# Performance work log

Measured on AMD Instinct MI355X. Metric: run time of the kernel, lower is better.

Reference implementation:

```python
import jax, jax.numpy as jnp
import numpy as np

N_NODES = 100000


def _graph_conv(x, W, b, src, dst, n_nodes):
    # DGL GraphConv, norm='both':
    #   h = x * out_deg(src)^{-1/2}; h = h @ W; agg = scatter_sum over dst;
    #   out = agg * in_deg(dst)^{-1/2} + b
    ones = jnp.ones(src.shape, dtype=x.dtype)
    out_deg = jax.ops.segment_sum(ones, src, num_segments=n_nodes)
    in_deg = jax.ops.segment_sum(ones, dst, num_segments=n_nodes)
    norm_src = jax.lax.rsqrt(jnp.maximum(out_deg, 1.0))  # [N]
    norm_dst = jax.lax.rsqrt(jnp.maximum(in_deg, 1.0))   # [N]
    h = (x * norm_src[:, None]) @ W                      # [N, hid]
    msgs = h[src]                                        # [E, hid] gather
    agg = jax.ops.segment_sum(msgs, dst, num_segments=n_nodes)  # [N, hid]
    return jax.nn.relu(agg * norm_dst[:, None] + b)


def setup_inputs() -> dict:
    key = jax.random.key(0)
    k1, k2, k3, k4, k5 = jax.random.split(key, 5)
    n, e, d = N_NODES, 1600000, 128
    x = jax.random.normal(k1, (n, d), dtype=jnp.float32)
    src = jax.random.randint(k2, (e,), 0, n, dtype=jnp.int32)
    dst = jax.random.randint(k3, (e,), 0, n, dtype=jnp.int32)
    # Xavier-ish init for GraphConv weights, zero bias (DGL default)
    W1 = jax.random.normal(k4, (d, d), dtype=jnp.float32) / np.sqrt(d)
    W2 = jax.random.normal(k5, (d, d), dtype=jnp.float32) / np.sqrt(d)
    b1 = jnp.zeros((d,), dtype=jnp.float32)
    b2 = jnp.zeros((d,), dtype=jnp.float32)
    return {"x": x, "W1": W1, "b1": b1, "W2": W2, "b2": b2, "src": src, "dst": dst}


def reference(x, W1, b1, W2, b2, src, dst):
    h = _graph_conv(x, W1, b1, src, dst, N_NODES)
    h = _graph_conv(h, W2, b2, src, dst, N_NODES)
    return h
```

## Files before the change

kernel.cpp:

```cpp
#include <hip/hip_runtime.h>
#include <hip/hip_fp16.h>

#define HD 128
#define CHUNK 4096
#define MAXNB 512

typedef _Float16 f16x8 __attribute__((ext_vector_type(8)));
typedef float f32x4 __attribute__((ext_vector_type(4)));

__global__ __launch_bounds__(256) void hist_count(const int* __restrict__ src,
                                                  const int* __restrict__ dst,
                                                  unsigned int* __restrict__ cnt4s,
                                                  unsigned int* __restrict__ gHist,
                                                  int N, int NB, int NC, int E) {
    __shared__ unsigned int hist[MAXNB];
    for (int b = threadIdx.x; b < NB; b += 256) hist[b] = 0;
    __syncthreads();
    int base = blockIdx.x * CHUNK;
    int e0 = base + 4 * threadIdx.x;
#pragma unroll
    for (int it = 0; it < CHUNK / 1024; ++it, e0 += 1024) {
        if (e0 + 3 < E) {
            int4 s4 = *(const int4*)(src + e0);
            int4 d4 = *(const int4*)(dst + e0);
            atomicAdd(&cnt4s[0 * N + s4.x], 1u);
            atomicAdd(&cnt4s[1 * N + s4.y], 1u);
            atomicAdd(&cnt4s[2 * N + s4.z], 1u);
            atomicAdd(&cnt4s[3 * N + s4.w], 1u);
            atomicAdd(&hist[d4.x >> 8], 1u);
            atomicAdd(&hist[d4.y >> 8], 1u);
            atomicAdd(&hist[d4.z >> 8], 1u);
            atomicAdd(&hist[d4.w >> 8], 1u);
        } else {
            for (int j = 0; j < 4; ++j)
                if (e0 + j < E) {
                    atomicAdd(&cnt4s[j * N + src[e0 + j]], 1u);
                    atomicAdd(&hist[dst[e0 + j] >> 8], 1u);
                }
        }
    }
    __syncthreads();
    for (int b = threadIdx.x; b < NB; b += 256)
        gHist[(size_t)b * NC + blockIdx.x] = hist[b];
}

__global__ __launch_bounds__(256) void make_norm_src(const unsigned int* __restrict__ cnt4s,
                                                     float* __restrict__ norm_src, int N) {
    int i = blockIdx.x * 256 + threadIdx.x;
    if (i < N) {
        float od = (float)(cnt4s[i] + cnt4s[N + i] + cnt4s[2 * N + i] + cnt4s[3 * N + i]);
        norm_src[i] = rsqrtf(od > 1.f ? od : 1.f);
    }
}

__global__ __launch_bounds__(256) void prep_w(const float* __restrict__ W1,
                                              const float* __restrict__ W2,
                                              _Float16* __restrict__ Wt) {
    const float* W = blockIdx.x ? W2 : W1;
    _Float16* T = Wt + (size_t)blockIdx.x * HD * HD;
    for (int i = threadIdx.x; i < HD * HD; i += 256) {
        int k = i >> 7, c = i & 127;
        T[c * HD + k] = (_Float16)W[i];
    }
}

__global__ __launch_bounds__(256) void scan_a(const unsigned int* __restrict__ cnt,
                                              unsigned int* __restrict__ excl,
                                              unsigned int* __restrict__ bsum, int n) {
    int i = blockIdx.x * 256 + threadIdx.x;
    unsigned int v = (i < n) ? cnt[i] : 0u;
    unsigned int x = v;
#pragma unroll
    for (int d = 1; d < 64; d <<= 1) {
        unsigned int y = __shfl_up(x, d, 64);
        if ((threadIdx.x & 63) >= d) x += y;
    }
    __shared__ unsigned int wsum[4];
    if ((threadIdx.x & 63) == 63) wsum[threadIdx.x >> 6] = x;
    __syncthreads();
    unsigned int woff = 0;
    for (int w = 0; w < (int)(threadIdx.x >> 6); ++w) woff += wsum[w];
    unsigned int incl = x + woff;
    if (i < n) excl[i] = incl - v;
    if (threadIdx.x == 255) bsum[blockIdx.x] = incl;
}

__global__ __launch_bounds__(1024) void scan_b(const unsigned int* __restrict__ bsum,
                                               unsigned int* __restrict__ boff, int nb) {
    int t = threadIdx.x;
    unsigned int v = (t < nb) ? bsum[t] : 0u;
    unsigned int x = v;
#pragma unroll
    for (int d = 1; d < 64; d <<= 1) {
        unsigned int y = __shfl_up(x, d, 64);
        if ((t & 63) >= d) x += y;
    }
    __shared__ unsigned int wsum[16];
    if ((t & 63) == 63) wsum[t >> 6] = x;
    __syncthreads();
    unsigned int woff = 0;
    for (int w = 0; w < (t >> 6); ++w) woff += wsum[w];
    unsigned int incl = x + woff;
    if (t < nb) boff[t] = incl - v;
}

__global__ __launch_bounds__(256) void scan_c(unsigned int* __restrict__ excl,
                                              const unsigned int* __restrict__ boff, int n) {
    int i = blockIdx.x * 256 + threadIdx.x;
    if (i < n) excl[i] += boff[blockIdx.x];
}

__global__ __launch_bounds__(256) void scatter_coarse(const int* __restrict__ src,
                                                      const int* __restrict__ dst,
                                                      const unsigned int* __restrict__ scanA,
                                                      unsigned int* __restrict__ packed,
                                                      int NB, int NC, int E) {
    __shared__ unsigned int curs[MAXNB];
    int chunk = blockIdx.x;
    for (int b = threadIdx.x; b < NB; b += 256)
        curs[b] = scanA[(size_t)b * NC + chunk];
    __syncthreads();
    int base = chunk * CHUNK;
    int end = base + CHUNK < E ? base + CHUNK : E;
    for (int e = base + threadIdx.x; e < end; e += 256) {
        int d = dst[e];
        int s = src[e];
        unsigned int pos = atomicAdd(&curs[d >> 8], 1u);
        packed[pos] = ((unsigned int)(d & 255) << 24) | (unsigned int)s;
    }
}

__global__ __launch_bounds__(256) void fine_sort(const unsigned int* __restrict__ packed,
                                                 const unsigned int* __restrict__ scanA,
                                                 int* __restrict__ sorted_src,
                                                 unsigned int* __restrict__ offsets,
                                                 unsigned int* __restrict__ cntg,
                                                 float* __restrict__ normd,
                                                 int NB, int NC, int N, int E) {
    __shared__ unsigned int cnt[256];
    __shared__ unsigned int curs[256];
    __shared__ unsigned int wsum[4];
    int b = blockIdx.x;
    int t = threadIdx.x;
    unsigned int S = scanA[(size_t)b * NC];
    unsigned int T = (b + 1 < NB) ? scanA[(size_t)(b + 1) * NC] : (unsigned int)E;
    cnt[t] = 0;
    __syncthreads();
    for (unsigned int j = S + t; j < T; j += 256)
        atomicAdd(&cnt[packed[j] >> 24], 1u);
    __syncthreads();
    unsigned int v = cnt[t], x = v;
    int lane = t & 63;
#pragma unroll
    for (int d = 1; d < 64; d <<= 1) {
        unsigned int y = __shfl_up(x, d, 64);
        if (lane >= d) x += y;
    }
    if (lane == 63) wsum[t >> 6] = x;
    __syncthreads();
    unsigned int woff = 0;
    for (int w = 0; w < (t >> 6); ++w) woff += wsum[w];
    unsigned int ex = x - v + woff;
    curs[t] = ex;
    int node = b * 256 + t;
    if (node < N) {
        offsets[node] = S + ex;
        cntg[node] = v;
        float f = (float)v;
        normd[node] = rsqrtf(f > 1.f ? f : 1.f);
    }
    __syncthreads();
    for (unsigned int j = S + t; j < T; j += 256) {
        unsigned int p = packed[j];
        unsigned int pos = S + atomicAdd(&curs[p >> 24], 1u);
        sorted_src[pos] = (int)(p & 0xFFFFFFu);
    }
}

__global__ __launch_bounds__(256) void prep_x(const float* __restrict__ x,
                                              const float* __restrict__ norm,
                                              _Float16* __restrict__ xh, int total) {
    int t = blockIdx.x * 256 + threadIdx.x;
    if (t >= total) return;
    int row = t >> 5;
    float nr = norm[row];
    float4 v = ((const float4*)x)[t];
    __half2 lo = __floats2half2_rn(v.x * nr, v.y * nr);
    __half2 hi = __floats2half2_rn(v.z * nr, v.w * nr);
    uint2 pk;
    pk.x = *(unsigned int*)&lo;
    pk.y = *(unsigned int*)&hi;
    ((uint2*)xh)[t] = pk;
}

__global__ __launch_bounds__(256) void gemm_mfma(const _Float16* __restrict__ xh,
                                                 const _Float16* __restrict__ Wt,
                                                 _Float16* __restrict__ h, int n) {
    const int tid = threadIdx.x;
    const int w  = tid >> 6;
    const int l  = tid & 63;
    const int lg = l >> 4;
    const int li = l & 15;
    const int m  = blockIdx.x * 64 + w * 16 + li;

    const _Float16* xrow = xh + (size_t)m * HD + lg * 8;
    f16x8 xf[4];
#pragma unroll
    for (int kk = 0; kk < 4; ++kk)
        xf[kk] = *(const f16x8*)(xrow + kk * 32);

    f32x4 acc[8];
#pragma unroll
    for (int t = 0; t < 8; ++t) acc[t] = (f32x4){0.f, 0.f, 0.f, 0.f};

#pragma unroll
    for (int t = 0; t < 8; ++t) {
        const _Float16* wrow = Wt + (size_t)(t * 16 + li) * HD + lg * 8;
#pragma unroll
        for (int kk = 0; kk < 4; ++kk) {
            f16x8 wf = *(const f16x8*)(wrow + kk * 32);
            acc[t] = __builtin_amdgcn_mfma_f32_16x16x32_f16(wf, xf[kk], acc[t], 0, 0, 0);
        }
    }

    if (m < n) {
        _Float16* hp = h + (size_t)m * HD + lg * 4;
#pragma unroll
        for (int t = 0; t < 8; ++t) {
            __half2 p0 = __floats2half2_rn(acc[t][0], acc[t][1]);
            __half2 p1 = __floats2half2_rn(acc[t][2], acc[t][3]);
            uint2 pk;
            pk.x = *(unsigned int*)&p0;
            pk.y = *(unsigned int*)&p1;
            *(uint2*)(hp + t * 16) = pk;
        }
    }
}

template <bool MID>
__global__ __launch_bounds__(256) void aggregate_k(const __half* __restrict__ h,
                                                   const int* __restrict__ sorted_src,
                                                   const unsigned int* __restrict__ offsets,
                                                   const unsigned int* __restrict__ cnt,
                                                   const float* __restrict__ norm_dst,
                                                   const float* __restrict__ nsrc,
                                                   const float* __restrict__ bias,
                                                   float* __restrict__ outF,
                                                   __half* __restrict__ outH, int n) {
    int node = blockIdx.x * 4 + (int)(threadIdx.x >> 6);
    if (node >= n) return;
    int lane = threadIdx.x & 63;
    int g   = lane >> 4;
    int sub = lane & 15;

    unsigned int start = offsets[node];
    unsigned int deg   = cnt[node];
    const int* sp = sorted_src + start;
    const uint4* h4 = (const uint4*)h;

    float acc[8];
#pragma unroll
    for (int j = 0; j < 8; ++j) acc[j] = 0.f;

#define ACCUM(u)                                                                  \
    { float2 f;                                                                   \
      f = __half22float2(*(const __half2*)&(u).x); acc[0] += f.x; acc[1] += f.y;  \
      f = __half22float2(*(const __half2*)&(u).y); acc[2] += f.x; acc[3] += f.y;  \
      f = __half22float2(*(const __half2*)&(u).z); acc[4] += f.x; acc[5] += f.y;  \
      f = __half22float2(*(const __half2*)&(u).w); acc[6] += f.x; acc[7] += f.y; }

    unsigned int i = 0;
    for (; i + 16 <= deg; i += 16) {
        int s0 = sp[i + g];
        int s1 = sp[i + 4 + g];
        int s2 = sp[i + 8 + g];
        int s3 = sp[i + 12 + g];
        uint4 u0 = h4[(size_t)s0 * 16 + sub];
        uint4 u1 = h4[(size_t)s1 * 16 + sub];
        uint4 u2 = h4[(size_t)s2 * 16 + sub];
        uint4 u3 = h4[(size_t)s3 * 16 + sub];
        ACCUM(u0);
        ACCUM(u1);
        ACCUM(u2);
        ACCUM(u3);
    }
    for (; i < deg; i += 4) {
        if (i + g < deg) {
            int s = sp[i + g];
            uint4 u = h4[(size_t)s * 16 + sub];
            ACCUM(u);
        }
    }
#undef ACCUM

#pragma unroll
    for (int j = 0; j < 8; ++j) {
        acc[j] += __shfl_xor(acc[j], 16, 64);
        acc[j] += __shfl_xor(acc[j], 32, 64);
    }

    float nd = norm_dst[node];
    int col2 = sub * 4 + g;
    float2 bb = ((const float2*)bias)[col2];
    float vx = fmaxf(fmaf(acc[g * 2 + 0], nd, bb.x), 0.f);
    float vy = fmaxf(fmaf(acc[g * 2 + 1], nd, bb.y), 0.f);
    if (MID) {
        float ns = nsrc[node];
        __half2 p = __floats2half2_rn(vx * ns, vy * ns);
        ((__half2*)outH)[(size_t)node * 64 + col2] = p;
    } else {
        ((float2*)outF)[(size_t)node * 64 + col2] = make_float2(vx, vy);
    }
}

extern "C" void kernel_launch(void* const* d_in, const int* in_sizes, int n_in,
                              void* d_out, int out_size, void* d_ws, size_t ws_size,
                              hipStream_t stream) {
    const float* x   = (const float*)d_in[0];
    const float* W1  = (const float*)d_in[1];
    const float* b1  = (const float*)d_in[2];
    const float* W2  = (const float*)d_in[3];
    const float* b2  = (const float*)d_in[4];
    const int*   src = (const int*)d_in[5];
    const int*   dst = (const int*)d_in[6];

    const int N = in_sizes[0] / HD;
    const int E = in_sizes[5];
    float* out = (float*)d_out;

    const int NP = (N + 63) & ~63;
    const int NB = (N + 255) / 256;
    const int NC = (E + CHUNK - 1) / CHUNK;
    const int scanLen = NB * NC;
    const int nbS = (scanLen + 255) / 256;
    const int nbN = (N + 255) / 256;

    float*        norm_src = (float*)d_ws;
    float*        normd    = norm_src + N;
    unsigned int* cntg     = (unsigned int*)(normd + N);
    unsigned int* offsets  = cntg + N;
    unsigned int* cnt4s    = offsets + N;
    unsigned int* gHist    = cnt4s + 4 * N;
    unsigned int* scanA    = gHist + scanLen;
    unsigned int* bsum     = scanA + scanLen;
    unsigned int* boff     = bsum + 1024;
    unsigned int* packed   = boff + 1024;
    int*          sorted   = (int*)(packed + E);
    _Float16*     h        = (_Float16*)(sorted + E);
    _Float16*     xh       = h + (size_t)NP * HD;
    _Float16*     Wt       = xh + (size_t)NP * HD;

    hipMemsetAsync(cnt4s, 0, (size_t)4 * N * 4, stream);
    prep_w<<<2, 256, 0, stream>>>(W1, W2, Wt);
    hist_count<<<NC, 256, 0, stream>>>(src, dst, cnt4s, gHist, N, NB, NC, E);
    make_norm_src<<<nbN, 256, 0, stream>>>(cnt4s, norm_src, N);
    scan_a<<<nbS, 256, 0, stream>>>(gHist, scanA, bsum, scanLen);
    scan_b<<<1, 1024, 0, stream>>>(bsum, boff, nbS);
    scan_c<<<nbS, 256, 0, stream>>>(scanA, boff, scanLen);
    scatter_coarse<<<NC, 256, 0, stream>>>(src, dst, scanA, packed, NB, NC, E);
    fine_sort<<<NB, 256, 0, stream>>>(packed, scanA, sorted, offsets, cntg, normd, NB, NC, N, E);

    prep_x<<<(N * 32 + 255) / 256, 256, 0, stream>>>(x, norm_src, xh, N * 32);
    gemm_mfma<<<NP / 64, 256, 0, stream>>>(xh, Wt, h, N);
    aggregate_k<true><<<(N + 3) / 4, 256, 0, stream>>>((const __half*)h, sorted, offsets, cntg,
                                                       normd, norm_src, b1, nullptr,
                                                       (__half*)xh, N);

    gemm_mfma<<<NP / 64, 256, 0, stream>>>(xh, Wt + HD * HD, h, N);
    aggregate_k<false><<<(N + 3) / 4, 256, 0, stream>>>((const __half*)h, sorted, offsets, cntg,
                                                        normd, nullptr, b2, out, nullptr, N);
}
```

Before: 369.7 us.

## Store hidden features in column slices and aggregate per node-slice thread

The GEMM now writes h in a sliced layout of eight 16-column panels, and aggregation assigns one thread per node per slice, gathering 32-byte fragments and accumulating in packed fp16. This removes cross-lane shuffle reductions and aims to improve cache locality of the random gathers per slice. It trades fp32 accumulation for fp16, which adds rounding error, and each thread now walks its neighbor list serially with uncoalesced index reads.

```diff
diff --git a/kernel.cpp b/kernel.cpp
--- a/kernel.cpp
+++ b/kernel.cpp
@@ -195,7 +195,7 @@
 
 __global__ __launch_bounds__(256) void gemm_mfma(const _Float16* __restrict__ xh,
                                                  const _Float16* __restrict__ Wt,
-                                                 _Float16* __restrict__ h, int n) {
+                                                 _Float16* __restrict__ h, int NP, int n) {
     const int tid = threadIdx.x;
     const int w  = tid >> 6;
     const int l  = tid & 63;
@@ -224,7 +224,6 @@
     }
 
     if (m < n) {
-        _Float16* hp = h + (size_t)m * HD + lg * 4;
 #pragma unroll
         for (int t = 0; t < 8; ++t) {
             __half2 p0 = __floats2half2_rn(acc[t][0], acc[t][1]);
@@ -232,84 +231,76 @@
             uint2 pk;
             pk.x = *(unsigned int*)&p0;
             pk.y = *(unsigned int*)&p1;
-            *(uint2*)(hp + t * 16) = pk;
+            *(uint2*)(h + ((size_t)t * NP + m) * 16 + lg * 4) = pk;
         }
     }
 }
 
 template <bool MID>
-__global__ __launch_bounds__(256) void aggregate_k(const __half* __restrict__ h,
-                                                   const int* __restrict__ sorted_src,
-                                                   const unsigned int* __restrict__ offsets,
-                                                   const unsigned int* __restrict__ cnt,
-                                                   const float* __restrict__ norm_dst,
-                                                   const float* __restrict__ nsrc,
-                                                   const float* __restrict__ bias,
-                                                   float* __restrict__ outF,
-                                                   __half* __restrict__ outH, int n) {
-    int node = blockIdx.x * 4 + (int)(threadIdx.x >> 6);
+__global__ __launch_bounds__(256) void aggregate_slice(const _Float16* __restrict__ h,
+                                                       const int* __restrict__ sorted_src,
+                                                       const unsigned int* __restrict__ offsets,
+                                                       const unsigned int* __restrict__ cnt,
+                                                       const float* __restrict__ norm_dst,
+                                                       const float* __restrict__ nsrc,
+                                                       const float* __restrict__ bias,
+                                                       float* __restrict__ outF,
+                                                       _Float16* __restrict__ outH,
+                                                       int NP, int n) {
+    const int slice = blockIdx.x & 7;
+    const int node  = (blockIdx.x >> 3) * 256 + threadIdx.x;
     if (node >= n) return;
-    int lane = threadIdx.x & 63;
-    int g   = lane >> 4;
-    int sub = lane & 15;
-
-    unsigned int start = offsets[node];
-    unsigned int deg   = cnt[node];
-    const int* sp = sorted_src + start;
-    const uint4* h4 = (const uint4*)h;
-
-    float acc[8];
-#pragma unroll
-    for (int j = 0; j < 8; ++j) acc[j] = 0.f;
-
-#define ACCUM(u)                                                                  \
-    { float2 f;                                                                   \
-      f = __half22float2(*(const __half2*)&(u).x); acc[0] += f.x; acc[1] += f.y;  \
-      f = __half22float2(*(const __half2*)&(u).y); acc[2] += f.x; acc[3] += f.y;  \
-      f = __half22float2(*(const __half2*)&(u).z); acc[4] += f.x; acc[5] += f.y;  \
-      f = __half22float2(*(const __half2*)&(u).w); acc[6] += f.x; acc[7] += f.y; }
-
+
+    const _Float16* hs = h + (size_t)slice * NP * 16;
+    unsigned int off = offsets[node];
+    unsigned int deg = cnt[node];
+    const int* sp = sorted_src + off;
+
+    f16x8 a0 = {}, a1 = {}, b0 = {}, b1 = {};
     unsigned int i = 0;
-    for (; i + 16 <= deg; i += 16) {
-        int s0 = sp[i + g];
-        int s1 = sp[i + 4 + g];
-        int s2 = sp[i + 8 + g];
-        int s3 = sp[i + 12 + g];
-        uint4 u0 = h4[(size_t)s0 * 16 + sub];
-        uint4 u1 = h4[(size_t)s1 * 16 + sub];
-        uint4 u2 = h4[(size_t)s2 * 16 + sub];
-        uint4 u3 = h4[(size_t)s3 * 16 + sub];
-        ACCUM(u0);
-        ACCUM(u1);
-        ACCUM(u2);
-        ACCUM(u3);
-    }
-    for (; i < deg; i += 4) {
-        if (i + g < deg) {
-            int s = sp[i + g];
-            uint4 u = h4[(size_t)s * 16 + sub];
-            ACCUM(u);
-        }
-    }
-#undef ACCUM
-
+    for (; i + 2 <= deg; i += 2) {
+        int s0 = sp[i];
+        int s1 = sp[i + 1];
+        const f16x8* r0 = (const f16x8*)(hs + (size_t)s0 * 16);
+        const f16x8* r1 = (const f16x8*)(hs + (size_t)s1 * 16);
+        a0 += r0[0];
+        a1 += r0[1];
+        b0 += r1[0];
+        b1 += r1[1];
+    }
+    if (i < deg) {
+        int s = sp[i];
+        const f16x8* r = (const f16x8*)(hs + (size_t)s * 16);
+        a0 += r[0];
+        a1 += r[1];
+    }
+    a0 += b0;
+    a1 += b1;
+
+    float nd = norm_dst[node];
+    const float* bp = bias + slice * 16;
+    float f[16];
 #pragma unroll
     for (int j = 0; j < 8; ++j) {
-        acc[j] += __shfl_xor(acc[j], 16, 64);
-        acc[j] += __shfl_xor(acc[j], 32, 64);
-    }
-
-    float nd = norm_dst[node];
-    int col2 = sub * 4 + g;
-    float2 bb = ((const float2*)bias)[col2];
-    float vx = fmaxf(fmaf(acc[g * 2 + 0], nd, bb.x), 0.f);
-    float vy = fmaxf(fmaf(acc[g * 2 + 1], nd, bb.y), 0.f);
+        f[j]     = fmaxf(fmaf((float)a0[j], nd, bp[j]), 0.f);
+        f[8 + j] = fmaxf(fmaf((float)a1[j], nd, bp[8 + j]), 0.f);
+    }
     if (MID) {
         float ns = nsrc[node];
-        __half2 p = __floats2half2_rn(vx * ns, vy * ns);
-        ((__half2*)outH)[(size_t)node * 64 + col2] = p;
+        f16x8 w0, w1;
+#pragma unroll
+        for (int j = 0; j < 8; ++j) {
+            w0[j] = (_Float16)(f[j] * ns);
+            w1[j] = (_Float16)(f[8 + j] * ns);
+        }
+        _Float16* op = outH + (size_t)node * HD + slice * 16;
+        *(f16x8*)op = w0;
+        *(f16x8*)(op + 8) = w1;
     } else {
-        ((float2*)outF)[(size_t)node * 64 + col2] = make_float2(vx, vy);
+        float* op = outF + (size_t)node * HD + slice * 16;
+#pragma unroll
+        for (int q = 0; q < 4; ++q)
+            *(float4*)(op + q * 4) = make_float4(f[q * 4], f[q * 4 + 1], f[q * 4 + 2], f[q * 4 + 3]);
     }
 }
 
@@ -334,6 +325,7 @@
     const int scanLen = NB * NC;
     const int nbS = (scanLen + 255) / 256;
     const int nbN = (N + 255) / 256;
+    const int aggGrid = 8 * ((N + 255) / 256);
 
     float*        norm_src = (float*)d_ws;
     float*        normd    = norm_src + N;
@@ -361,12 +353,11 @@
     fine_sort<<<NB, 256, 0, stream>>>(packed, scanA, sorted, offsets, cntg, normd, NB, NC, N, E);
 
     prep_x<<<(N * 32 + 255) / 256, 256, 0, stream>>>(x, norm_src, xh, N * 32);
-    gemm_mfma<<<NP / 64, 256, 0, stream>>>(xh, Wt, h, N);
-    aggregate_k<true><<<(N + 3) / 4, 256, 0, stream>>>((const __half*)h, sorted, offsets, cntg,
-                                                       normd, norm_src, b1, nullptr,
-                                                       (__half*)xh, N);
-
-    gemm_mfma<<<NP / 64, 256, 0, stream>>>(xh, Wt + HD * HD, h, N);
-    aggregate_k<false><<<(N + 3) / 4, 256, 0, stream>>>((const __half*)h, sorted, offsets, cntg,
-                                                        normd, nullptr, b2, out, nullptr, N);
-}
+    gemm_mfma<<<NP / 64, 256, 0, stream>>>(xh, Wt, h, NP, N);
+    aggregate_slice<true><<<aggGrid, 256, 0, stream>>>(h, sorted, offsets, cntg, normd,
+                                                       norm_src, b1, nullptr, xh, NP, N);
+
+    gemm_mfma<<<NP / 64, 256, 0, stream>>>(xh, Wt + HD * HD, h, NP, N);
+    aggregate_slice<false><<<aggGrid, 256, 0, stream>>>(h, sorted, offsets, cntg, normd,
+                                                        nullptr, b2, out, nullptr, NP, N);
+}
```

Measured after the change: 496.6 us. 1.34x slower.

## Move out-degree counting into scatter pass and fuse x normalization into first GEMM

Applied to the files above, without the earlier changes.

The src out-degree atomics move from the histogram kernel into the coarse scatter kernel, so the histogram pass reads only dst. The scatter kernel now uses vectorized int4 loads. The separate prep_x pass is removed: a new GEMM variant reads fp32 x, scales it by norm_src and converts it to fp16 in registers, which avoids writing and re-reading an fp16 copy. CHUNK doubles to 8192, which halves the number of chunk blocks and the size of the histogram scan in exchange for less parallelism per pass.

```diff
diff --git a/kernel.cpp b/kernel.cpp
--- a/kernel.cpp
+++ b/kernel.cpp
@@ -2,21 +2,116 @@
 #include <hip/hip_fp16.h>
 
 #define HD 128
-#define CHUNK 4096
+#define CHUNK 8192
 #define MAXNB 512
 
 typedef _Float16 f16x8 __attribute__((ext_vector_type(8)));
 typedef float f32x4 __attribute__((ext_vector_type(4)));
 
-__global__ __launch_bounds__(256) void hist_count(const int* __restrict__ src,
-                                                  const int* __restrict__ dst,
-                                                  unsigned int* __restrict__ cnt4s,
-                                                  unsigned int* __restrict__ gHist,
-                                                  int N, int NB, int NC, int E) {
+__global__ __launch_bounds__(256) void hist_coarse(const int* __restrict__ dst,
+                                                   unsigned int* __restrict__ gHist,
+                                                   int NB, int NC, int E) {
     __shared__ unsigned int hist[MAXNB];
     for (int b = threadIdx.x; b < NB; b += 256) hist[b] = 0;
     __syncthreads();
     int base = blockIdx.x * CHUNK;
+    int e0 = base + 4 * threadIdx.x;
+#pragma unroll
+    for (int it = 0; it < CHUNK / 1024; ++it, e0 += 1024) {
+        if (e0 + 3 < E) {
+            int4 d4 = *(const int4*)(dst + e0);
+            atomicAdd(&hist[d4.x >> 8], 1u);
+            atomicAdd(&hist[d4.y >> 8], 1u);
+            atomicAdd(&hist[d4.z >> 8], 1u);
+            atomicAdd(&hist[d4.w >> 8], 1u);
+        } else {
+            for (int j = 0; j < 4; ++j)
+                if (e0 + j < E) atomicAdd(&hist[dst[e0 + j] >> 8], 1u);
+        }
+    }
+    __syncthreads();
+    for (int b = threadIdx.x; b < NB; b += 256)
+        gHist[(size_t)b * NC + blockIdx.x] = hist[b];
+}
+
+__global__ __launch_bounds__(256) void make_norm_src(const unsigned int* __restrict__ cnt4s,
+                                                     float* __restrict__ norm_src, int N) {
+    int i = blockIdx.x * 256 + threadIdx.x;
+    if (i < N) {
+        float od = (float)(cnt4s[i] + cnt4s[N + i] + cnt4s[2 * N + i] + cnt4s[3 * N + i]);
+        norm_src[i] = rsqrtf(od > 1.f ? od : 1.f);
+    }
+}
+
+__global__ __launch_bounds__(256) void prep_w(const float* __restrict__ W1,
+                                              const float* __restrict__ W2,
+                                              _Float16* __restrict__ Wt) {
+    const float* W = blockIdx.x ? W2 : W1;
+    _Float16* T = Wt + (size_t)blockIdx.x * HD * HD;
+    for (int i = threadIdx.x; i < HD * HD; i += 256) {
+        int k = i >> 7, c = i & 127;
+        T[c * HD + k] = (_Float16)W[i];
+    }
+}
+
+__global__ __launch_bounds__(256) void scan_a(const unsigned int* __restrict__ cnt,
+                                              unsigned int* __restrict__ excl,
+                                              unsigned int* __restrict__ bsum, int n) {
+    int i = blockIdx.x * 256 + threadIdx.x;
+    unsigned int v = (i < n) ? cnt[i] : 0u;
+    unsigned int x = v;
+#pragma unroll
+    for (int d = 1; d < 64; d <<= 1) {
+        unsigned int y = __shfl_up(x, d, 64);
+        if ((threadIdx.x & 63) >= d) x += y;
+    }
+    __shared__ unsigned int wsum[4];
+    if ((threadIdx.x & 63) == 63) wsum[threadIdx.x >> 6] = x;
+    __syncthreads();
+    unsigned int woff = 0;
+    for (int w = 0; w < (int)(threadIdx.x >> 6); ++w) woff += wsum[w];
+    unsigned int incl = x + woff;
+    if (i < n) excl[i] = incl - v;
+    if (threadIdx.x == 255) bsum[blockIdx.x] = incl;
+}
+
+__global__ __launch_bounds__(1024) void scan_b(const unsigned int* __restrict__ bsum,
+                                               unsigned int* __restrict__ boff, int nb) {
+    int t = threadIdx.x;
+    unsigned int v = (t < nb) ? bsum[t] : 0u;
+    unsigned int x = v;
+#pragma unroll
+    for (int d = 1; d < 64; d <<= 1) {
+        unsigned int y = __shfl_up(x, d, 64);
+        if ((t & 63) >= d) x += y;
+    }
+    __shared__ unsigned int wsum[16];
+    if ((t & 63) == 63) wsum[t >> 6] = x;
+    __syncthreads();
+    unsigned int woff = 0;
+    for (int w = 0; w < (t >> 6); ++w) woff += wsum[w];
+    unsigned int incl = x + woff;
+    if (t < nb) boff[t] = incl - v;
+}
+
+__global__ __launch_bounds__(256) void scan_c(unsigned int* __restrict__ excl,
+                                              const unsigned int* __restrict__ boff, int n) {
+    int i = blockIdx.x * 256 + threadIdx.x;
+    if (i < n) excl[i] += boff[blockIdx.x];
+}
+
+__global__ __launch_bounds__(256) void scatter_coarse(const int* __restrict__ src,
+                                                      const int* __restrict__ dst,
+                                                      const unsigned int* __restrict__ scanA,
+                                                      unsigned int* __restrict__ packed,
+                                                      unsigned int* __restrict__ cnt4s,
+                                                      int N, int NB, int NC, int E) {
+    __shared__ unsigned int curs[MAXNB];
+    int chunk = blockIdx.x;
+    for (int b = threadIdx.x; b < NB; b += 256)
+        curs[b] = scanA[(size_t)b * NC + chunk];
+    __syncthreads();
+    int base = chunk * CHUNK;
     int e0 = base + 4 * threadIdx.x;
 #pragma unroll
     for (int it = 0; it < CHUNK / 1024; ++it, e0 += 1024) {
@@ -27,106 +122,23 @@
             atomicAdd(&cnt4s[1 * N + s4.y], 1u);
             atomicAdd(&cnt4s[2 * N + s4.z], 1u);
             atomicAdd(&cnt4s[3 * N + s4.w], 1u);
-            atomicAdd(&hist[d4.x >> 8], 1u);
-            atomicAdd(&hist[d4.y >> 8], 1u);
-            atomicAdd(&hist[d4.z >> 8], 1u);
-            atomicAdd(&hist[d4.w >> 8], 1u);
+            unsigned int p0 = atomicAdd(&curs[d4.x >> 8], 1u);
+            unsigned int p1 = atomicAdd(&curs[d4.y >> 8], 1u);
+            unsigned int p2 = atomicAdd(&curs[d4.z >> 8], 1u);
+            unsigned int p3 = atomicAdd(&curs[d4.w >> 8], 1u);
+            packed[p0] = ((unsigned int)(d4.x & 255) << 24) | (unsigned int)s4.x;
+            packed[p1] = ((unsigned int)(d4.y & 255) << 24) | (unsigned int)s4.y;
+            packed[p2] = ((unsigned int)(d4.z & 255) << 24) | (unsigned int)s4.z;
+            packed[p3] = ((unsigned int)(d4.w & 255) << 24) | (unsigned int)s4.w;
         } else {
             for (int j = 0; j < 4; ++j)
                 if (e0 + j < E) {
-                    atomicAdd(&cnt4s[j * N + src[e0 + j]], 1u);
-                    atomicAdd(&hist[dst[e0 + j] >> 8], 1u);
+                    int d = dst[e0 + j], s = src[e0 + j];
+                    atomicAdd(&cnt4s[j * N + s], 1u);
+                    unsigned int pos = atomicAdd(&curs[d >> 8], 1u);
+                    packed[pos] = ((unsigned int)(d & 255) << 24) | (unsigned int)s;
                 }
         }
-    }
-    __syncthreads();
-    for (int b = threadIdx.x; b < NB; b += 256)
-        gHist[(size_t)b * NC + blockIdx.x] = hist[b];
-}
-
-__global__ __launch_bounds__(256) void make_norm_src(const unsigned int* __restrict__ cnt4s,
-                                                     float* __restrict__ norm_src, int N) {
-    int i = blockIdx.x * 256 + threadIdx.x;
-    if (i < N) {
-        float od = (float)(cnt4s[i] + cnt4s[N + i] + cnt4s[2 * N + i] + cnt4s[3 * N + i]);
-        norm_src[i] = rsqrtf(od > 1.f ? od : 1.f);
-    }
-}
-
-__global__ __launch_bounds__(256) void prep_w(const float* __restrict__ W1,
-                                              const float* __restrict__ W2,
-                                              _Float16* __restrict__ Wt) {
-    const float* W = blockIdx.x ? W2 : W1;
-    _Float16* T = Wt + (size_t)blockIdx.x * HD * HD;
-    for (int i = threadIdx.x; i < HD * HD; i += 256) {
-        int k = i >> 7, c = i & 127;
-        T[c * HD + k] = (_Float16)W[i];
-    }
-}
-
-__global__ __launch_bounds__(256) void scan_a(const unsigned int* __restrict__ cnt,
-                                              unsigned int* __restrict__ excl,
-                                              unsigned int* __restrict__ bsum, int n) {
-    int i = blockIdx.x * 256 + threadIdx.x;
-    unsigned int v = (i < n) ? cnt[i] : 0u;
-    unsigned int x = v;
-#pragma unroll
-    for (int d = 1; d < 64; d <<= 1) {
-        unsigned int y = __shfl_up(x, d, 64);
-        if ((threadIdx.x & 63) >= d) x += y;
-    }
-    __shared__ unsigned int wsum[4];
-    if ((threadIdx.x & 63) == 63) wsum[threadIdx.x >> 6] = x;
-    __syncthreads();
-    unsigned int woff = 0;
-    for (int w = 0; w < (int)(threadIdx.x >> 6); ++w) woff += wsum[w];
-    unsigned int incl = x + woff;
-    if (i < n) excl[i] = incl - v;
-    if (threadIdx.x == 255) bsum[blockIdx.x] = incl;
-}
-
-__global__ __launch_bounds__(1024) void scan_b(const unsigned int* __restrict__ bsum,
-                                               unsigned int* __restrict__ boff, int nb) {
-    int t = threadIdx.x;
-    unsigned int v = (t < nb) ? bsum[t] : 0u;
-    unsigned int x = v;
-#pragma unroll
-    for (int d = 1; d < 64; d <<= 1) {
-        unsigned int y = __shfl_up(x, d, 64);
-        if ((t & 63) >= d) x += y;
-    }
-    __shared__ unsigned int wsum[16];
-    if ((t & 63) == 63) wsum[t >> 6] = x;
-    __syncthreads();
-    unsigned int woff = 0;
-    for (int w = 0; w < (t >> 6); ++w) woff += wsum[w];
-    unsigned int incl = x + woff;
-    if (t < nb) boff[t] = incl - v;
-}
-
-__global__ __launch_bounds__(256) void scan_c(unsigned int* __restrict__ excl,
-                                              const unsigned int* __restrict__ boff, int n) {
-    int i = blockIdx.x * 256 + threadIdx.x;
-    if (i < n) excl[i] += boff[blockIdx.x];
-}
-
-__global__ __launch_bounds__(256) void scatter_coarse(const int* __restrict__ src,
-                                                      const int* __restrict__ dst,
-                                                      const unsigned int* __restrict__ scanA,
-                                                      unsigned int* __restrict__ packed,
-                                                      int NB, int NC, int E) {
-    __shared__ unsigned int curs[MAXNB];
-    int chunk = blockIdx.x;
-    for (int b = threadIdx.x; b < NB; b += 256)
-        curs[b] = scanA[(size_t)b * NC + chunk];
-    __syncthreads();
-    int base = chunk * CHUNK;
-    int end = base + CHUNK < E ? base + CHUNK : E;
-    for (int e = base + threadIdx.x; e < end; e += 256) {
-        int d = dst[e];
-        int s = src[e];
-        unsigned int pos = atomicAdd(&curs[d >> 8], 1u);
-        packed[pos] = ((unsigned int)(d & 255) << 24) | (unsigned int)s;
     }
 }
 
@@ -177,20 +189,63 @@
     }
 }
 
-__global__ __launch_bounds__(256) void prep_x(const float* __restrict__ x,
-                                              const float* __restrict__ norm,
-                                              _Float16* __restrict__ xh, int total) {
-    int t = blockIdx.x * 256 + threadIdx.x;
-    if (t >= total) return;
-    int row = t >> 5;
-    float nr = norm[row];
-    float4 v = ((const float4*)x)[t];
-    __half2 lo = __floats2half2_rn(v.x * nr, v.y * nr);
-    __half2 hi = __floats2half2_rn(v.z * nr, v.w * nr);
-    uint2 pk;
-    pk.x = *(unsigned int*)&lo;
-    pk.y = *(unsigned int*)&hi;
-    ((uint2*)xh)[t] = pk;
+__global__ __launch_bounds__(256) void gemm_mfma_f32(const float* __restrict__ x,
+                                                     const float* __restrict__ norm,
+                                                     const _Float16* __restrict__ Wt,
+                                                     _Float16* __restrict__ h, int n) {
+    const int tid = threadIdx.x;
+    const int w  = tid >> 6;
+    const int l  = tid & 63;
+    const int lg = l >> 4;
+    const int li = l & 15;
+    const int m  = blockIdx.x * 64 + w * 16 + li;
+
+    f16x8 xf[4];
+    if (m < n) {
+        float nr = norm[m];
+        const float* xrow = x + (size_t)m * HD + lg * 8;
+#pragma unroll
+        for (int kk = 0; kk < 4; ++kk) {
+            float4 a = *(const float4*)(xrow + kk * 32);
+            float4 b = *(const float4*)(xrow + kk * 32 + 4);
+            f16x8 v;
+            v[0] = (_Float16)(a.x * nr); v[1] = (_Float16)(a.y * nr);
+            v[2] = (_Float16)(a.z * nr); v[3] = (_Float16)(a.w * nr);
+            v[4] = (_Float16)(b.x * nr); v[5] = (_Float16)(b.y * nr);
+            v[6] = (_Float16)(b.z * nr); v[7] = (_Float16)(b.w * nr);
+            xf[kk] = v;
+        }
+    } else {
+#pragma unroll
+        for (int kk = 0; kk < 4; ++kk) xf[kk] = (f16x8){};
+    }
+
+    f32x4 acc[8];
+#pragma unroll
+    for (int t = 0; t < 8; ++t) acc[t] = (f32x4){0.f, 0.f, 0.f, 0.f};
+
+#pragma unroll
+    for (int t = 0; t < 8; ++t) {
+        const _Float16* wrow = Wt + (size_t)(t * 16 + li) * HD + lg * 8;
+#pragma unroll
+        for (int kk = 0; kk < 4; ++kk) {
+            f16x8 wf = *(const f16x8*)(wrow + kk * 32);
+            acc[t] = __builtin_amdgcn_mfma_f32_16x16x32_f16(wf, xf[kk], acc[t], 0, 0, 0);
+        }
+    }
+
+    if (m < n) {
+        _Float16* hp = h + (size_t)m * HD + lg * 4;
+#pragma unroll
+        for (int t = 0; t < 8; ++t) {
+            __half2 p0 = __floats2half2_rn(acc[t][0], acc[t][1]);
+            __half2 p1 = __floats2half2_rn(acc[t][2], acc[t][3]);
+            uint2 pk;
+            pk.x = *(unsigned int*)&p0;
+            pk.y = *(unsigned int*)&p1;
+            *(uint2*)(hp + t * 16) = pk;
+        }
+    }
 }
 
 __global__ __launch_bounds__(256) void gemm_mfma(const _Float16* __restrict__ xh,
@@ -352,16 +407,15 @@
 
     hipMemsetAsync(cnt4s, 0, (size_t)4 * N * 4, stream);
     prep_w<<<2, 256, 0, stream>>>(W1, W2, Wt);
-    hist_count<<<NC, 256, 0, stream>>>(src, dst, cnt4s, gHist, N, NB, NC, E);
-    make_norm_src<<<nbN, 256, 0, stream>>>(cnt4s, norm_src, N);
+    hist_coarse<<<NC, 256, 0, stream>>>(dst, gHist, NB, NC, E);
     scan_a<<<nbS, 256, 0, stream>>>(gHist, scanA, bsum, scanLen);
     scan_b<<<1, 1024, 0, stream>>>(bsum, boff, nbS);
     scan_c<<<nbS, 256, 0, stream>>>(scanA, boff, scanLen);
-    scatter_coarse<<<NC, 256, 0, stream>>>(src, dst, scanA, packed, NB, NC, E);
+    scatter_coarse<<<NC, 256, 0, stream>>>(src, dst, scanA, packed, cnt4s, N, NB, NC, E);
+    make_norm_src<<<nbN, 256, 0, stream>>>(cnt4s, norm_src, N);
     fine_sort<<<NB, 256, 0, stream>>>(packed, scanA, sorted, offsets, cntg, normd, NB, NC, N, E);
 
-    prep_x<<<(N * 32 + 255) / 256, 256, 0, stream>>>(x, norm_src, xh, N * 32);
-    gemm_mfma<<<NP / 64, 256, 0, stream>>>(xh, Wt, h, N);
+    gemm_mfma_f32<<<NP / 64, 256, 0, stream>>>(x, norm_src, Wt, h, N);
     aggregate_k<true><<<(N + 3) / 4, 256, 0, stream>>>((const __half*)h, sorted, offsets, cntg,
                                                        normd, norm_src, b1, nullptr,
                                                        (__half*)xh, N);
```

Result: faster. 352.0 us (-4.8%).
